# Kernel tuning notes

Measured on AMD Instinct MI355X. Metric: run time of the kernel, lower is better.

Reference implementation:

```python
import jax, jax.numpy as jnp
import numpy as np
from jax import lax

FRAMES, BATCH, IN_DIM = 512, 2048, 84
HIDDEN, OUT_DIM = 300, 10


def setup_inputs() -> dict:
    key = jax.random.key(0)
    k1, k2, k3, k4 = jax.random.split(key, 4)
    hand_data = jax.random.normal(k1, (FRAMES, BATCH, IN_DIM), dtype=jnp.float32)
    hidden_state = jnp.zeros((BATCH, HIDDEN), dtype=jnp.float32)
    # Linear weights (PyTorch convention: y = x @ W.T), Kaiming-uniform-ish scale
    Wi = jax.random.normal(k2, (HIDDEN, IN_DIM), dtype=jnp.float32) / np.sqrt(IN_DIM)
    Wh = jax.random.normal(k3, (HIDDEN, HIDDEN), dtype=jnp.float32) / np.sqrt(HIDDEN)
    Wo = jax.random.normal(k4, (OUT_DIM, HIDDEN), dtype=jnp.float32) / np.sqrt(HIDDEN)
    return {"hand_data": hand_data, "hidden_state": hidden_state,
            "Wi": Wi, "Wh": Wh, "Wo": Wo}


def reference(hand_data, hidden_state, Wi, Wh, Wo):
    # Precompute the input projection for all frames in one big GEMM:
    # [F,B,I] x [H,I] -> [F,B,H]
    x_proj = jnp.einsum('fbi,hi->fbh', hand_data, Wi)

    def step(h, xp):
        # Elman cell: h' = tanh(i2h(x) + h2h(h))
        h = jnp.tanh(xp + h @ Wh.T)
        return h, None

    h_final, _ = lax.scan(step, hidden_state, x_proj)
    # h2o is computed every iteration in the original, but only the last
    # value is returned, so computing it once on the final hidden state
    # yields identical output.
    out = h_final @ Wo.T  # [B, OUT_DIM]
    return out, h_final
```

## Files before the change

kernel.cpp:

```cpp
#include <hip/hip_runtime.h>
#include <hip/hip_bf16.h>

#define FRAMES 512
#define BATCH 2048
#define IN_DIM 84
#define HIDDEN 300
#define OUT_DIM 10

#define MT 16
#define HROW 512
#define XOFF 8192
#define XROW 512
#define BUFB 16384
#define KFH 5
#define KFX 3
#define NT 3

#define L2E2 2.88539008177792681f

typedef __attribute__((ext_vector_type(8))) short s8v;
typedef __attribute__((ext_vector_type(4))) short s4v;
typedef __attribute__((ext_vector_type(4))) float f4v;
typedef __attribute__((ext_vector_type(4))) int   i4v;

__device__ __forceinline__ short f2b(float x) {
    __hip_bfloat16 h = __float2bfloat16(x);
    return *reinterpret_cast<short*>(&h);
}
__device__ __forceinline__ void lgkm_barrier() {
    asm volatile("s_waitcnt lgkmcnt(0)" ::: "memory");
    __builtin_amdgcn_s_barrier();
}


#define MFI(T, K, ACC) ACC = __builtin_amdgcn_mfma_i32_16x16x64_i8(wq[T][K], bh[K], ACC, 0, 0, 0)
#define MFX(T, K, ACC) ACC = __builtin_amdgcn_mfma_f32_16x16x32_bf16(wx[T][K], bx[K], ACC, 0, 0, 0)
#define TAIL(AI, AF, IDX) do { unsigned b_[4];                                  \
        _Pragma("unroll")                                                       \
        for (int r_ = 0; r_ < 4; ++r_) {                                        \
            float z2_ = fmaf(qs2885, (float)AI[r_], AF[r_]);                    \
            float ex_ = __builtin_amdgcn_exp2f(z2_);                            \
            b_[r_] = __float_as_uint(                                           \
                fmaf(-254.f, __builtin_amdgcn_rcpf(ex_ + 1.f), 12583039.f));    \
        }                                                                       \
        unsigned t0_ = __builtin_amdgcn_perm(b_[1], b_[0], 0x00000400u);        \
        unsigned t1_ = __builtin_amdgcn_perm(b_[3], b_[2], 0x00000400u);        \
        unsigned pk_ = __builtin_amdgcn_perm(t1_, t0_, 0x05040100u);            \
        *(unsigned*)&ldsb[IDX] = pk_; } while (0)

__global__ __launch_bounds__(512, 2)
void rnn_kernel(const float* __restrict__ x, const float* __restrict__ h0,
                const float* __restrict__ Wi, const float* __restrict__ Wh,
                const float* __restrict__ Wo, float* __restrict__ out)
{
    __shared__ __align__(16) char ldsb[2 * BUFB];
    __shared__ float redbuf[8];
    const int tid  = threadIdx.x;
    const int lane = tid & 63;
    const int wv   = tid >> 6;
    const int l15  = lane & 15;
    const int lkhi = lane >> 4;
    const int b0   = blockIdx.x * MT;
    const bool w3  = (wv < 3);

    float m = 0.f;
    for (int i = tid; i < HIDDEN * HIDDEN; i += 512)
        m = fmaxf(m, fabsf(Wh[i]));
#pragma unroll
    for (int o = 32; o; o >>= 1) m = fmaxf(m, __shfl_xor(m, o));
    if (lane == 0) redbuf[wv] = m;
    __syncthreads();
    float gm = 0.f;
#pragma unroll
    for (int i = 0; i < 8; ++i) gm = fmaxf(gm, redbuf[i]);
    const float inv_sw = 127.f / gm;
    const float qs2885 = (gm / (127.f * 127.f)) * L2E2;

    i4v wq[NT][KFH];
    s8v wx[NT][KFX];
#pragma unroll
    for (int i = 0; i < NT; ++i) {
        const int n = (wv + 8 * i) * 16 + l15;
#pragma unroll
        for (int kf = 0; kf < KFH; ++kf) {
            int dw0 = 0, dw1 = 0, dw2 = 0, dw3 = 0;
#pragma unroll
            for (int j = 0; j < 16; ++j) {
                int k = kf * 64 + lkhi * 16 + j;
                float f = (n < HIDDEN && k < HIDDEN) ? Wh[n * HIDDEN + k] : 0.f;
                int q = (int)rintf(f * inv_sw) & 255;
                if ((j >> 2) == 0) dw0 |= q << ((j & 3) * 8);
                else if ((j >> 2) == 1) dw1 |= q << ((j & 3) * 8);
                else if ((j >> 2) == 2) dw2 |= q << ((j & 3) * 8);
                else dw3 |= q << ((j & 3) * 8);
            }
            wq[i][kf] = (i4v){dw0, dw1, dw2, dw3};
        }
#pragma unroll
        for (int f = 0; f < KFX; ++f) {
            s8v v;
#pragma unroll
            for (int j = 0; j < 8; ++j) {
                int k = f * 32 + lkhi * 8 + j;
                v[j] = f2b((n < HIDDEN && k < IN_DIM) ? L2E2 * Wi[n * IN_DIM + k] : 0.f);
            }
            wx[i][f] = v;
        }
    }

    {
        i4v z = (i4v){0, 0, 0, 0};
        for (int i = tid; i < 2 * BUFB / 16; i += 512)
            ((i4v*)ldsb)[i] = z;
    }
    __syncthreads();

    for (int i = tid; i < MT * HIDDEN; i += 512) {
        int r = i / HIDDEN, c = i % HIDDEN;
        float h = h0[(size_t)(b0 + r) * HIDDEN + c];
        ldsb[r * HROW + ((r & 7) << 4) + c] =
            (char)(__float_as_uint(fmaf(h, 127.f, 12582912.f)) & 255u);
    }
    if (tid < 336) {
        const float4* xs = reinterpret_cast<const float4*>(x + (size_t)b0 * IN_DIM);
        float4 v0 = xs[tid];
        int r = tid / 21, c = tid % 21;
        s4v pk = {f2b(v0.x), f2b(v0.y), f2b(v0.z), f2b(v0.w)};
        *reinterpret_cast<s4v*>(&ldsb[XOFF + r * XROW + ((r & 7) << 4) + c * 8]) = pk;
    }

    const int hrd = l15 * HROW + ((l15 & 7) << 4) + lkhi * 16;
    const int hwr = l15 * HROW + ((l15 & 7) << 4) + lkhi * 4;
    const int xrd = XOFF + l15 * XROW + ((l15 & 7) << 4) + lkhi * 16;
    const int xti = (tid < 336) ? tid : 0;
    const int xr_ = xti / 21, xc_ = xti % 21;
    const int xcb = XOFF + xr_ * XROW + ((xr_ & 7) << 4) + xc_ * 8;
    const bool xact = (tid < 336);
    const f4v zero4 = (f4v){0.f, 0.f, 0.f, 0.f};
    const i4v zeroi = (i4v){0, 0, 0, 0};

    float4 xa0, xb0;
    xa0 = reinterpret_cast<const float4*>(x + ((size_t)BATCH + b0) * IN_DIM)[xti];
    __syncthreads();

#define STEP(PH, SF, A0, B0, LOADF, COMMITF)                                    \
    {                                                                           \
        if (LOADF) {                                                            \
            B0 = reinterpret_cast<const float4*>(                               \
                x + ((size_t)((SF) + 2) * BATCH + b0) * IN_DIM)[xti];           \
        }                                                                       \
        if ((COMMITF) && xact) {                                                \
            s4v pk = {f2b(A0.x), f2b(A0.y), f2b(A0.z), f2b(A0.w)};              \
            *(s4v*)&ldsb[((PH) ^ 1) * BUFB + xcb] = pk;                         \
        }                                                                       \
        i4v bh[KFH]; s8v bx[KFX];                                               \
        _Pragma("unroll")                                                       \
        for (int kf = 0; kf < KFH; ++kf)                                        \
            bh[kf] = *(const i4v*)&ldsb[(PH) * BUFB + hrd + kf * 64];           \
        _Pragma("unroll")                                                       \
        for (int f = 0; f < KFX; ++f)                                           \
            bx[f] = *(const s8v*)&ldsb[(PH) * BUFB + xrd + f * 64];             \
        __builtin_amdgcn_s_setprio(1);                                          \
        if (w3) {                                                               \
            i4v a0i = __builtin_amdgcn_mfma_i32_16x16x64_i8(wq[0][0], bh[0], zeroi, 0, 0, 0); \
            i4v a1i = __builtin_amdgcn_mfma_i32_16x16x64_i8(wq[1][0], bh[0], zeroi, 0, 0, 0); \
            i4v a2i = __builtin_amdgcn_mfma_i32_16x16x64_i8(wq[2][0], bh[0], zeroi, 0, 0, 0); \
            _Pragma("unroll")                                                   \
            for (int kf = 1; kf < KFH; ++kf) {                                  \
                MFI(0, kf, a0i); MFI(1, kf, a1i); MFI(2, kf, a2i);              \
            }                                                                   \
            f4v a0f = __builtin_amdgcn_mfma_f32_16x16x32_bf16(wx[0][0], bx[0], zero4, 0, 0, 0); \
            f4v a1f = __builtin_amdgcn_mfma_f32_16x16x32_bf16(wx[1][0], bx[0], zero4, 0, 0, 0); \
            f4v a2f = __builtin_amdgcn_mfma_f32_16x16x32_bf16(wx[2][0], bx[0], zero4, 0, 0, 0); \
            _Pragma("unroll")                                                   \
            for (int f = 1; f < KFX; ++f) {                                     \
                MFX(0, f, a0f); MFX(1, f, a1f); MFX(2, f, a2f);                 \
            }                                                                   \
            __builtin_amdgcn_s_setprio(0);                                      \
            TAIL(a0i, a0f, ((PH) ^ 1) * BUFB + hwr + (wv) * 16);                \
            TAIL(a1i, a1f, ((PH) ^ 1) * BUFB + hwr + (wv + 8) * 16);            \
            TAIL(a2i, a2f, ((PH) ^ 1) * BUFB + hwr + (wv + 16) * 16);           \
        } else {                                                                \
            i4v a0i = __builtin_amdgcn_mfma_i32_16x16x64_i8(wq[0][0], bh[0], zeroi, 0, 0, 0); \
            i4v a1i = __builtin_amdgcn_mfma_i32_16x16x64_i8(wq[1][0], bh[0], zeroi, 0, 0, 0); \
            _Pragma("unroll")                                                   \
            for (int kf = 1; kf < KFH; ++kf) {                                  \
                MFI(0, kf, a0i); MFI(1, kf, a1i);                               \
            }                                                                   \
            f4v a0f = __builtin_amdgcn_mfma_f32_16x16x32_bf16(wx[0][0], bx[0], zero4, 0, 0, 0); \
            f4v a1f = __builtin_amdgcn_mfma_f32_16x16x32_bf16(wx[1][0], bx[0], zero4, 0, 0, 0); \
            _Pragma("unroll")                                                   \
            for (int f = 1; f < KFX; ++f) {                                     \
                MFX(0, f, a0f); MFX(1, f, a1f);                                 \
            }                                                                   \
            __builtin_amdgcn_s_setprio(0);                                      \
            TAIL(a0i, a0f, ((PH) ^ 1) * BUFB + hwr + (wv) * 16);                \
            TAIL(a1i, a1f, ((PH) ^ 1) * BUFB + hwr + (wv + 8) * 16);            \
        }                                                                       \
        lgkm_barrier();                                                         \
    }

    for (int s = 0; s < FRAMES - 2; s += 2) {
        STEP(0, s,     xa0, xb0, 1, 1)
        STEP(1, s + 1, xb0, xa0, 1, 1)
    }
    STEP(0, 510, xa0, xb0, 0, 1)
    STEP(1, 511, xb0, xa0, 0, 0)
#undef STEP

    const float dq = 1.f / 127.f;
    float* hout = out + BATCH * OUT_DIM;
    for (int i = tid; i < MT * HIDDEN; i += 512) {
        int r = i / HIDDEN, c = i % HIDDEN;
        hout[(size_t)(b0 + r) * HIDDEN + c] =
            (float)((int)(signed char)ldsb[r * HROW + ((r & 7) << 4) + c]) * dq;
    }
    if (tid < MT * OUT_DIM) {
        int r = tid / OUT_DIM, c = tid % OUT_DIM;
        float sum = 0.f;
        for (int k = 0; k < HIDDEN; ++k) {
            float h = (float)((int)(signed char)ldsb[r * HROW + ((r & 7) << 4) + k]) * dq;
            sum = fmaf(h, Wo[c * HIDDEN + k], sum);
        }
        out[(b0 + r) * OUT_DIM + c] = sum;
    }
}

extern "C" void kernel_launch(void* const* d_in, const int* in_sizes, int n_in,
                              void* d_out, int out_size, void* d_ws, size_t ws_size,
                              hipStream_t stream) {
    const float* x  = (const float*)d_in[0];
    const float* h0 = (const float*)d_in[1];
    const float* Wi = (const float*)d_in[2];
    const float* Wh = (const float*)d_in[3];
    const float* Wo = (const float*)d_in[4];
    float* out = (float*)d_out;
    rnn_kernel<<<dim3(BATCH / MT), dim3(512), 0, stream>>>(x, h0, Wi, Wh, Wo, out);
}
```

Measured before the change: 475.0 us.

## Load x directly into MFMA B-operand registers instead of staging through LDS

Each lane now loads its own x fragment from global memory straight into registers and converts it to bf16 with packed v_cvt_pk_bf16_f32, instead of cooperatively staging bf16 x through shared memory. This removes the per-step LDS write and the three LDS reads of x, and halves the LDS buffer size. In exchange it issues six redundant, less coalesced global loads per lane per step, with only a one-step prefetch distance. Load latency that is not hidden could stall the serial recurrence.

Measured after the change: 584.5 us. +23.1%, slower.

```diff
diff --git a/kernel.cpp b/kernel.cpp
--- a/kernel.cpp
+++ b/kernel.cpp
@@ -9,17 +9,13 @@
 
 #define MT 16
 #define HROW 512
-#define XOFF 8192
-#define XROW 512
-#define BUFB 16384
+#define BUFB 8192
 #define KFH 5
-#define KFX 3
 #define NT 3
 
 #define L2E2 2.88539008177792681f
 
 typedef __attribute__((ext_vector_type(8))) short s8v;
-typedef __attribute__((ext_vector_type(4))) short s4v;
 typedef __attribute__((ext_vector_type(4))) float f4v;
 typedef __attribute__((ext_vector_type(4))) int   i4v;
 
@@ -31,10 +27,18 @@
     asm volatile("s_waitcnt lgkmcnt(0)" ::: "memory");
     __builtin_amdgcn_s_barrier();
 }
+__device__ __forceinline__ s8v cvtpk8(float4 a, float4 b) {
+    unsigned u0, u1, u2, u3;
+    asm("v_cvt_pk_bf16_f32 %0, %1, %2" : "=v"(u0) : "v"(a.x), "v"(a.y));
+    asm("v_cvt_pk_bf16_f32 %0, %1, %2" : "=v"(u1) : "v"(a.z), "v"(a.w));
+    asm("v_cvt_pk_bf16_f32 %0, %1, %2" : "=v"(u2) : "v"(b.x), "v"(b.y));
+    asm("v_cvt_pk_bf16_f32 %0, %1, %2" : "=v"(u3) : "v"(b.z), "v"(b.w));
+    i4v t = (i4v){(int)u0, (int)u1, (int)u2, (int)u3};
+    return *(s8v*)&t;
+}
 
 
 #define MFI(T, K, ACC) ACC = __builtin_amdgcn_mfma_i32_16x16x64_i8(wq[T][K], bh[K], ACC, 0, 0, 0)
-#define MFX(T, K, ACC) ACC = __builtin_amdgcn_mfma_f32_16x16x32_bf16(wx[T][K], bx[K], ACC, 0, 0, 0)
 #define TAIL(AI, AF, IDX) do { unsigned b_[4];                                  \
         _Pragma("unroll")                                                       \
         for (int r_ = 0; r_ < 4; ++r_) {                                        \
@@ -77,7 +81,7 @@
     const float qs2885 = (gm / (127.f * 127.f)) * L2E2;
 
     i4v wq[NT][KFH];
-    s8v wx[NT][KFX];
+    s8v wx0[NT], wx1[NT], wx2[NT];
 #pragma unroll
     for (int i = 0; i < NT; ++i) {
         const int n = (wv + 8 * i) * 16 + l15;
@@ -97,14 +101,14 @@
             wq[i][kf] = (i4v){dw0, dw1, dw2, dw3};
         }
 #pragma unroll
-        for (int f = 0; f < KFX; ++f) {
+        for (int f = 0; f < 3; ++f) {
             s8v v;
 #pragma unroll
             for (int j = 0; j < 8; ++j) {
                 int k = f * 32 + lkhi * 8 + j;
                 v[j] = f2b((n < HIDDEN && k < IN_DIM) ? L2E2 * Wi[n * IN_DIM + k] : 0.f);
             }
-            wx[i][f] = v;
+            if (f == 0) wx0[i] = v; else if (f == 1) wx1[i] = v; else wx2[i] = v;
         }
     }
 
@@ -121,45 +125,37 @@
         ldsb[r * HROW + ((r & 7) << 4) + c] =
             (char)(__float_as_uint(fmaf(h, 127.f, 12582912.f)) & 255u);
     }
-    if (tid < 336) {
-        const float4* xs = reinterpret_cast<const float4*>(x + (size_t)b0 * IN_DIM);
-        float4 v0 = xs[tid];
-        int r = tid / 21, c = tid % 21;
-        s4v pk = {f2b(v0.x), f2b(v0.y), f2b(v0.z), f2b(v0.w)};
-        *reinterpret_cast<s4v*>(&ldsb[XOFF + r * XROW + ((r & 7) << 4) + c * 8]) = pk;
-    }
 
     const int hrd = l15 * HROW + ((l15 & 7) << 4) + lkhi * 16;
     const int hwr = l15 * HROW + ((l15 & 7) << 4) + lkhi * 4;
-    const int xrd = XOFF + l15 * XROW + ((l15 & 7) << 4) + lkhi * 16;
-    const int xti = (tid < 336) ? tid : 0;
-    const int xr_ = xti / 21, xc_ = xti % 21;
-    const int xcb = XOFF + xr_ * XROW + ((xr_ & 7) << 4) + xc_ * 8;
-    const bool xact = (tid < 336);
     const f4v zero4 = (f4v){0.f, 0.f, 0.f, 0.f};
     const i4v zeroi = (i4v){0, 0, 0, 0};
 
-    float4 xa0, xb0;
-    xa0 = reinterpret_cast<const float4*>(x + ((size_t)BATCH + b0) * IN_DIM)[xti];
+    const float* xp = x + (size_t)(b0 + l15) * IN_DIM;
+    const int o00 = lkhi * 8,      o01 = lkhi * 8 + 4;
+    const int o10 = 32 + lkhi * 8, o11 = 36 + lkhi * 8;
+    const int o20 = (lkhi < 3) ? 64 + lkhi * 8 : 0;
+    const int o21 = (lkhi < 2) ? 68 + lkhi * 8 : 0;
+
+    float4 xf0, xf1, xf2, xf3, xf4, xf5;
+    xf0 = *(const float4*)(xp + o00); xf1 = *(const float4*)(xp + o01);
+    xf2 = *(const float4*)(xp + o10); xf3 = *(const float4*)(xp + o11);
+    xf4 = *(const float4*)(xp + o20); xf5 = *(const float4*)(xp + o21);
+    s8v bx0 = cvtpk8(xf0, xf1), bx1 = cvtpk8(xf2, xf3), bx2 = cvtpk8(xf4, xf5);
     __syncthreads();
 
-#define STEP(PH, SF, A0, B0, LOADF, COMMITF)                                    \
+#define STEP(PH, SF, LOADF)                                                     \
     {                                                                           \
         if (LOADF) {                                                            \
-            B0 = reinterpret_cast<const float4*>(                               \
-                x + ((size_t)((SF) + 2) * BATCH + b0) * IN_DIM)[xti];           \
-        }                                                                       \
-        if ((COMMITF) && xact) {                                                \
-            s4v pk = {f2b(A0.x), f2b(A0.y), f2b(A0.z), f2b(A0.w)};              \
-            *(s4v*)&ldsb[((PH) ^ 1) * BUFB + xcb] = pk;                         \
-        }                                                                       \
-        i4v bh[KFH]; s8v bx[KFX];                                               \
+            const float* r_ = xp + (size_t)((SF) + 1) * (BATCH * IN_DIM);       \
+            xf0 = *(const float4*)(r_ + o00); xf1 = *(const float4*)(r_ + o01); \
+            xf2 = *(const float4*)(r_ + o10); xf3 = *(const float4*)(r_ + o11); \
+            xf4 = *(const float4*)(r_ + o20); xf5 = *(const float4*)(r_ + o21); \
+        }                                                                       \
+        i4v bh[KFH];                                                            \
         _Pragma("unroll")                                                       \
         for (int kf = 0; kf < KFH; ++kf)                                        \
             bh[kf] = *(const i4v*)&ldsb[(PH) * BUFB + hrd + kf * 64];           \
-        _Pragma("unroll")                                                       \
-        for (int f = 0; f < KFX; ++f)                                           \
-            bx[f] = *(const s8v*)&ldsb[(PH) * BUFB + xrd + f * 64];             \
         __builtin_amdgcn_s_setprio(1);                                          \
         if (w3) {                                                               \
             i4v a0i = __builtin_amdgcn_mfma_i32_16x16x64_i8(wq[0][0], bh[0], zeroi, 0, 0, 0); \
@@ -169,13 +165,15 @@
             for (int kf = 1; kf < KFH; ++kf) {                                  \
                 MFI(0, kf, a0i); MFI(1, kf, a1i); MFI(2, kf, a2i);              \
             }                                                                   \
-            f4v a0f = __builtin_amdgcn_mfma_f32_16x16x32_bf16(wx[0][0], bx[0], zero4, 0, 0, 0); \
-            f4v a1f = __builtin_amdgcn_mfma_f32_16x16x32_bf16(wx[1][0], bx[0], zero4, 0, 0, 0); \
-            f4v a2f = __builtin_amdgcn_mfma_f32_16x16x32_bf16(wx[2][0], bx[0], zero4, 0, 0, 0); \
-            _Pragma("unroll")                                                   \
-            for (int f = 1; f < KFX; ++f) {                                     \
-                MFX(0, f, a0f); MFX(1, f, a1f); MFX(2, f, a2f);                 \
-            }                                                                   \
+            f4v a0f = __builtin_amdgcn_mfma_f32_16x16x32_bf16(wx0[0], bx0, zero4, 0, 0, 0); \
+            f4v a1f = __builtin_amdgcn_mfma_f32_16x16x32_bf16(wx0[1], bx0, zero4, 0, 0, 0); \
+            f4v a2f = __builtin_amdgcn_mfma_f32_16x16x32_bf16(wx0[2], bx0, zero4, 0, 0, 0); \
+            a0f = __builtin_amdgcn_mfma_f32_16x16x32_bf16(wx1[0], bx1, a0f, 0, 0, 0); \
+            a1f = __builtin_amdgcn_mfma_f32_16x16x32_bf16(wx1[1], bx1, a1f, 0, 0, 0); \
+            a2f = __builtin_amdgcn_mfma_f32_16x16x32_bf16(wx1[2], bx1, a2f, 0, 0, 0); \
+            a0f = __builtin_amdgcn_mfma_f32_16x16x32_bf16(wx2[0], bx2, a0f, 0, 0, 0); \
+            a1f = __builtin_amdgcn_mfma_f32_16x16x32_bf16(wx2[1], bx2, a1f, 0, 0, 0); \
+            a2f = __builtin_amdgcn_mfma_f32_16x16x32_bf16(wx2[2], bx2, a2f, 0, 0, 0); \
             __builtin_amdgcn_s_setprio(0);                                      \
             TAIL(a0i, a0f, ((PH) ^ 1) * BUFB + hwr + (wv) * 16);                \
             TAIL(a1i, a1f, ((PH) ^ 1) * BUFB + hwr + (wv + 8) * 16);            \
@@ -187,25 +185,28 @@
             for (int kf = 1; kf < KFH; ++kf) {                                  \
                 MFI(0, kf, a0i); MFI(1, kf, a1i);                               \
             }                                                                   \
-            f4v a0f = __builtin_amdgcn_mfma_f32_16x16x32_bf16(wx[0][0], bx[0], zero4, 0, 0, 0); \
-            f4v a1f = __builtin_amdgcn_mfma_f32_16x16x32_bf16(wx[1][0], bx[0], zero4, 0, 0, 0); \
-            _Pragma("unroll")                                                   \
-            for (int f = 1; f < KFX; ++f) {                                     \
-                MFX(0, f, a0f); MFX(1, f, a1f);                                 \
-            }                                                                   \
+            f4v a0f = __builtin_amdgcn_mfma_f32_16x16x32_bf16(wx0[0], bx0, zero4, 0, 0, 0); \
+            f4v a1f = __builtin_amdgcn_mfma_f32_16x16x32_bf16(wx0[1], bx0, zero4, 0, 0, 0); \
+            a0f = __builtin_amdgcn_mfma_f32_16x16x32_bf16(wx1[0], bx1, a0f, 0, 0, 0); \
+            a1f = __builtin_amdgcn_mfma_f32_16x16x32_bf16(wx1[1], bx1, a1f, 0, 0, 0); \
+            a0f = __builtin_amdgcn_mfma_f32_16x16x32_bf16(wx2[0], bx2, a0f, 0, 0, 0); \
+            a1f = __builtin_amdgcn_mfma_f32_16x16x32_bf16(wx2[1], bx2, a1f, 0, 0, 0); \
             __builtin_amdgcn_s_setprio(0);                                      \
             TAIL(a0i, a0f, ((PH) ^ 1) * BUFB + hwr + (wv) * 16);                \
             TAIL(a1i, a1f, ((PH) ^ 1) * BUFB + hwr + (wv + 8) * 16);            \
         }                                                                       \
+        if (LOADF) {            \
+            bx0 = cvtpk8(xf0, xf1); bx1 = cvtpk8(xf2, xf3); bx2 = cvtpk8(xf4, xf5); \
+        }                                                                       \
         lgkm_barrier();                                                         \
     }
 
     for (int s = 0; s < FRAMES - 2; s += 2) {
-        STEP(0, s,     xa0, xb0, 1, 1)
-        STEP(1, s + 1, xb0, xa0, 1, 1)
-    }
-    STEP(0, 510, xa0, xb0, 0, 1)
-    STEP(1, 511, xb0, xa0, 0, 0)
+        STEP(0, s,     1)
+        STEP(1, s + 1, 1)
+    }
+    STEP(0, 510, 1)
+    STEP(1, 511, 0)
 #undef STEP
 
     const float dq = 1.f / 127.f;
```
